# Kernel tuning notes

Hardware: AMD Instinct MI355X
Metric: run time of the kernel (lower is better)

The kernel has to match this reference:

```python
import jax, jax.numpy as jnp
import numpy as np

PAD = 7                 # init padding
T = 2 * PAD + 1         # T_side_dense = 15 shifts per axis
LAMDA = 1.0             # init lamda
EPS = 1e-16             # hardcoded epsilon in the torch loss body


def _joint_hist(x_out, x_tf_out):
    # Equivalent of F.conv2d(x_out.permute(1,0,2,3), weight=x_tf_out.permute(1,0,2,3), padding=PAD)
    # expressed as T*T shifted matmuls (correlation / cost-volume form).
    bn, k, h, w = x_out.shape
    A = jnp.transpose(x_out, (1, 0, 2, 3))      # (k, bn, h, w)  conv "input"
    B = jnp.transpose(x_tf_out, (1, 0, 2, 3))   # (k, bn, h, w)  conv "weight"
    A_pad = jnp.pad(A, ((0, 0), (0, 0), (PAD, PAD), (PAD, PAD)))

    def step(carry, s):
        dy, dx = s // T, s % T
        sl = jax.lax.dynamic_slice(A_pad, (0, 0, dy, dx), (k, bn, h, w))
        # p[n, o] at this shift = sum_{c,y,x} A_pad[n,c,y+dy,x+dx] * B[o,c,y,x]
        return carry, jnp.einsum('nchw,ochw->no', sl, B)

    _, p = jax.lax.scan(step, None, jnp.arange(T * T))
    # (T*T, k, k) -> (T, T, k, k); matches torch p_i_j.permute(2, 3, 0, 1)
    return p.reshape(T, T, k, k)


def reference(x_out, x_tf_out):
    p = _joint_hist(x_out, x_tf_out)
    # shift to positive; min is detached in torch -> stop_gradient
    p = p - jax.lax.stop_gradient(p.min()) + EPS
    # normalize per shift over the (k, k) joint
    p = p / p.sum(axis=(2, 3), keepdims=True)
    # symmetrize
    p = (p + jnp.swapaxes(p, 2, 3)) / 2.0
    p_i = p.sum(axis=2, keepdims=True)   # (T, T, 1, k) marginal (broadcasts like repeat)
    p_j = p.sum(axis=3, keepdims=True)   # (T, T, k, 1) marginal
    loss = (-p * (jnp.log(p + EPS)
                  - LAMDA * jnp.log(p_i + EPS)
                  - LAMDA * jnp.log(p_j + EPS))).sum() / (T * T)
    return loss


def setup_inputs() -> dict:
    key = jax.random.key(0)
    k1, k2 = jax.random.split(key)
    bn, k, h, w = 16, 10, 224, 224
    # simplex over axis=1 is asserted by the torch module -> use softmax
    x_out = jax.nn.softmax(jax.random.normal(k1, (bn, k, h, w), dtype=jnp.float32), axis=1)
    x_tf_out = jax.nn.softmax(jax.random.normal(k2, (bn, k, h, w), dtype=jnp.float32), axis=1)
    return {"x_out": x_out, "x_tf_out": x_tf_out}
```

## Files before the change

### kernel.cpp

```cpp
#include <hip/hip_runtime.h>
#include <stdint.h>
#include <math.h>


#define PADV 7
#define TS 15
#define KCLS 10
#define HH 224
#define WW 224
#define MD 160
#define NCELL (MD*MD)
#define NBLK 256
#define TY 14
#define BSTRIDE 232
#define BPH 240
#define PLANEE 2408
#define ABUFE (8*PLANEE)
#define NRED 400
#define LEPS 1e-16

typedef __attribute__((ext_vector_type(4))) float f32x4;
typedef __attribute__((ext_vector_type(8))) short bf16x8;

__device__ __forceinline__ unsigned short f2bf(float f) {
  union { float f; uint32_t u; } v; v.f = f;
  return (unsigned short)((v.u + 0x7FFFu + ((v.u >> 16) & 1u)) >> 16);
}

__device__ __forceinline__ uint32_t pack2bf(float a, float b) {
  return (uint32_t)f2bf(a) | ((uint32_t)f2bf(b) << 16);
}

__device__ __forceinline__ void glds16(const unsigned short* g, unsigned short* l) {
  __builtin_amdgcn_global_load_lds(
      (const __attribute__((address_space(1))) unsigned int*)g,
      (__attribute__((address_space(3))) unsigned int*)l, 16, 0, 0);
}

__device__ __forceinline__ void plane_write(const f32x4 f[4], unsigned short* awr) {
  uint32_t w[8];
#pragma unroll
  for (int k = 0; k < 8; ++k)
    w[k] = pack2bf(f[k >> 1][(k & 1) * 2], f[k >> 1][(k & 1) * 2 + 1]);
#pragma unroll
  for (int c = 0; c < 8; ++c) {
    union { uint32_t u[4]; uint4 v; } o;
    if (c & 1) {
#pragma unroll
      for (int j = 0; j < 4; ++j) o.u[j] = w[j + (c + 1) / 2];
    } else {
#pragma unroll
      for (int j = 0; j < 4; ++j)
        o.u[j] = __builtin_amdgcn_alignbit(w[j + 1 + c / 2], w[j + c / 2], 16);
    }
    *(uint4*)(awr + c * PLANEE) = o.v;
  }
}

__global__ __launch_bounds__(256)
void prep_b(const float* __restrict__ xt, unsigned short* __restrict__ bp) {
  const int idx   = blockIdx.x * 256 + threadIdx.x;
  const int rowid = idx / 29;
  const int chunk = idx - rowid * 29;
  const int x0    = chunk * 8;
  const int yy    = rowid % BPH;
  const int cls   = rowid / BPH;
  const int row   = yy - PADV;
  union { unsigned short h[8]; uint4 v; } out;
  if (row >= 0 && row < HH && chunk < 28) {
    const float4* src = (const float4*)(xt + ((size_t)cls * HH + row) * WW + x0);
    const float4 f0 = src[0], f1 = src[1];
    out.h[0] = f2bf(f0.x); out.h[1] = f2bf(f0.y);
    out.h[2] = f2bf(f0.z); out.h[3] = f2bf(f0.w);
    out.h[4] = f2bf(f1.x); out.h[5] = f2bf(f1.y);
    out.h[6] = f2bf(f1.z); out.h[7] = f2bf(f1.w);
  } else {
    out.v = make_uint4(0u, 0u, 0u, 0u);
  }
  *(uint4*)(bp + (size_t)rowid * BSTRIDE + x0) = out.v;
}

__global__ __launch_bounds__(640, 3)
void corr_gemm(const float* __restrict__ xo, const unsigned short* __restrict__ bpad,
               float* __restrict__ partials) {
  __shared__ __align__(16) unsigned short ldsA8[2 * ABUFE];
  __shared__ __align__(16) unsigned short ldsB[KCLS * 16 * BSTRIDE];

  const int tid  = threadIdx.x;
  const int bid0 = blockIdx.x;
  const int bid  = (bid0 & 7) * 32 + (bid0 >> 3);
  const int b    = bid >> 4;
  const int y0   = (bid & 15) * TY;

  const int lane = tid & 63;
  const int wv   = tid >> 6;
  const int wm   = wv >> 1;
  const int wn   = wv & 1;
  const int quad = lane >> 4;
  const int l15  = lane & 15;

  f32x4 acc[2][5];
#pragma unroll
  for (int i = 0; i < 2; ++i)
#pragma unroll
    for (int j = 0; j < 5; ++j) acc[i][j] = (f32x4){0.f, 0.f, 0.f, 0.f};

  const float* Ab = xo + (size_t)b * KCLS * HH * WW;
  const unsigned short* Bb = bpad + (size_t)b * KCLS * BPH * BSTRIDE;

  const bool aw  = tid < 300;
  const int an   = aw ? tid / 30 : 0;
  const int atp  = aw ? tid - (tid / 30) * 30 : 0;
  const int axb  = atp * 8 - 8;
  bool gv[4];
#pragma unroll
  for (int g = 0; g < 4; ++g)
    gv[g] = aw && (axb + 4 * g >= 0) && (axb + 4 * g + 4 <= WW);
  unsigned short* const awr0 = ldsA8 + an * 240 + atp * 8;

  for (int pr = wv; pr < 15 * KCLS; pr += 10) {
    const int r15  = pr / KCLS;
    const int o    = pr - r15 * KCLS;
    const int yy   = y0 + r15;
    const int slot = (y0 - PADV + r15) & 15;
    if (lane < 29)
      glds16(Bb + ((size_t)o * BPH + yy) * BSTRIDE + lane * 8,
             ldsB + (o * 16 + slot) * BSTRIDE);
  }

  f32x4 f[4];
  {
    const float* src = Ab + ((size_t)an * HH + y0) * WW + axb;
#pragma unroll
    for (int g = 0; g < 4; ++g) {
      f[g] = (f32x4){0.f, 0.f, 0.f, 0.f};
      if (gv[g]) f[g] = *(const f32x4*)(src + 4 * g);
    }
  }
  if (aw) plane_write(f, awr0);
  __syncthreads();

  int cur = 0;
  for (int s = 0; s < TY; ++s) {
    const int y = y0 + s;
    const bool more = (s + 1 < TY);

    if (more) {
      const int yy   = y + 8 + PADV;
      const int slot = (y + 8) & 15;
      if (lane < 29)
        glds16(Bb + ((size_t)wv * BPH + yy) * BSTRIDE + lane * 8,
               ldsB + (wv * 16 + slot) * BSTRIDE);
      const float* src = Ab + ((size_t)an * HH + (y + 1)) * WW + axb;
#pragma unroll
      for (int g = 0; g < 4; ++g) {
        f[g] = (f32x4){0.f, 0.f, 0.f, 0.f};
        if (gv[g]) f[g] = *(const f32x4*)(src + 4 * g);
      }
    }

    const unsigned short* paB = ldsA8 + cur * ABUFE + (l15 & 7) * PLANEE + (l15 & 8);
    const int slotB = (y + PADV - l15) & 15;

#pragma unroll 1
    for (int xc = 0; xc < 7; ++xc) {
      const int x0 = xc * 32;
      bf16x8 afrag[2], bfrag[5];
#pragma unroll
      for (int mi = 0; mi < 2; ++mi)
        afrag[mi] = *(const bf16x8*)(paB + (wm * 2 + mi) * 240 + x0 + quad * 8);
#pragma unroll
      for (int ni = 0; ni < 5; ++ni) {
        const int to = wn * 5 + ni;
        bfrag[ni] = *(const bf16x8*)(ldsB + (to * 16 + slotB) * BSTRIDE + x0 + quad * 8);
      }
#pragma unroll
      for (int mi = 0; mi < 2; ++mi)
#pragma unroll
        for (int ni = 0; ni < 5; ++ni)
          acc[mi][ni] = __builtin_amdgcn_mfma_f32_16x16x32_bf16(
              afrag[mi], bfrag[ni], acc[mi][ni], 0, 0, 0);
    }

    if (more) {
      if (aw) plane_write(f, awr0 + (cur ^ 1) * ABUFE);
      __syncthreads();
      cur ^= 1;
    }
  }

  float* outp = partials + (size_t)bid * NCELL;
#pragma unroll
  for (int mi = 0; mi < 2; ++mi)
#pragma unroll
    for (int ni = 0; ni < 5; ++ni) {
      const int mrow = (wm * 2 + mi) * 16 + quad * 4;
      const int ncol = (wn * 5 + ni) * 16 + l15;
#pragma unroll
      for (int r = 0; r < 4; ++r)
        outp[(size_t)(mrow + r) * MD + ncol] = acc[mi][ni][r];
    }
}

__global__ __launch_bounds__(256)
void reduce_all(const float* __restrict__ partials, float* __restrict__ Cout,
                float* __restrict__ mins, float* __restrict__ dout) {
  const int tid = threadIdx.x;
  const int cl  = tid & 63;
  const int g   = tid >> 6;
  const int c   = blockIdx.x * 64 + cl;
  if (blockIdx.x == 0 && tid == 0) dout[0] = 0.f;

  const float* base = partials + (size_t)g * 64 * NCELL + c;
  double s0 = 0.0, s1 = 0.0, s2 = 0.0, s3 = 0.0;
  for (int p = 0; p < 64; p += 4) {
    s0 += (double)base[(size_t)(p + 0) * NCELL];
    s1 += (double)base[(size_t)(p + 1) * NCELL];
    s2 += (double)base[(size_t)(p + 2) * NCELL];
    s3 += (double)base[(size_t)(p + 3) * NCELL];
  }
  __shared__ double redd[256];
  redd[tid] = (s0 + s1) + (s2 + s3);
  __syncthreads();

  __shared__ float redm[64];
  if (tid < 64) {
    const double tot = redd[tid] + redd[tid + 64] + redd[tid + 128] + redd[tid + 192];
    const float sf = (float)tot;
    Cout[c] = sf;
    const int m  = c / MD;
    const int nn = c - m * MD;
    const bool valid = ((m & 15) < TS) && ((nn & 15) < TS);
    redm[tid] = valid ? sf : 3.4e38f;
  }
  __syncthreads();
  for (int st = 32; st > 0; st >>= 1) {
    if (tid < st) redm[tid] = fminf(redm[tid], redm[tid + st]);
    __syncthreads();
  }
  if (tid == 0) mins[blockIdx.x] = redm[0];
}

__global__ __launch_bounds__(128)
void loss_kernel(const float* __restrict__ Cmat, const float* __restrict__ mins,
                 float* __restrict__ dout) {
  const int s   = blockIdx.x;
  const int dy  = s / TS;
  const int dx  = s - dy * TS;
  const int tid = threadIdx.x;
  __shared__ float fm[128];
  __shared__ double q[100];
  __shared__ double sym[100];
  __shared__ double pi[10], pj[10];
  __shared__ double red[128];

  {
    float v = 3.4e38f;
    for (int i = tid; i < NRED; i += 128) v = fminf(v, mins[i]);
    fm[tid] = v;
  }
  __syncthreads();
  for (int st = 64; st > 0; st >>= 1) {
    if (tid < st) fm[tid] = fminf(fm[tid], fm[tid + st]);
    __syncthreads();
  }
  const double minv = (double)fm[0];
  __syncthreads();

  if (tid < 100) {
    const int n = tid / 10, o = tid - (tid / 10) * 10;
    const double v = (double)Cmat[(size_t)(n * 16 + dx) * MD + (o * 16 + dy)];
    q[tid] = v - minv + LEPS;
  }
  __syncthreads();
  red[tid] = (tid < 100) ? q[tid] : 0.0;
  __syncthreads();
  for (int st = 64; st > 0; st >>= 1) {
    if (tid < st) red[tid] += red[tid + st];
    __syncthreads();
  }
  const double Z = red[0];
  __syncthreads();
  if (tid < 100) {
    const int n = tid / 10, o = tid - (tid / 10) * 10;
    sym[tid] = (q[n * 10 + o] + q[o * 10 + n]) * 0.5 / Z;
  }
  __syncthreads();
  if (tid < 10) {
    double a = 0.0, bsum = 0.0;
    for (int n2 = 0; n2 < 10; ++n2) {
      a    += sym[n2 * 10 + tid];
      bsum += sym[tid * 10 + n2];
    }
    pi[tid] = a;
    pj[tid] = bsum;
  }
  __syncthreads();
  double term = 0.0;
  if (tid < 100) {
    const int n = tid / 10, o = tid - (tid / 10) * 10;
    const double sp = sym[tid];
    term = -sp * (log(sp + LEPS) - log(pi[o] + LEPS) - log(pj[n] + LEPS));
  }
  red[tid] = term;
  __syncthreads();
  for (int st = 64; st > 0; st >>= 1) {
    if (tid < st) red[tid] += red[tid + st];
    __syncthreads();
  }
  if (tid == 0) atomicAdd(dout, (float)(red[0] / (double)(TS * TS)));
}

extern "C" void kernel_launch(void* const* d_in, const int* in_sizes, int n_in,
                              void* d_out, int out_size, void* d_ws, size_t ws_size,
                              hipStream_t stream) {
  const float* xo = (const float*)d_in[0];
  const float* xt = (const float*)d_in[1];
  float* ws       = (float*)d_ws;

  float* partials = ws;
  float* Cmat     = partials + (size_t)NBLK * NCELL;
  float* mins     = Cmat + NCELL;
  unsigned short* bpad = (unsigned short*)(mins + 512);
  float* out      = (float*)d_out;

  hipLaunchKernelGGL(prep_b,      dim3(4350), dim3(256), 0, stream, xt, bpad);
  hipLaunchKernelGGL(corr_gemm,   dim3(NBLK), dim3(640), 0, stream, xo, bpad, partials);
  hipLaunchKernelGGL(reduce_all,  dim3(NRED), dim3(256), 0, stream, partials, Cmat, mins, out);
  hipLaunchKernelGGL(loss_kernel, dim3(225),  dim3(128), 0, stream, Cmat, mins, out);
}
```

Baseline: 148.7 us.

## Split correlation GEMM blocks across output-class halves and single-buffer A tile

The correlation GEMM now launches twice as many blocks with half the threads, each block covering only five of the ten output classes (an N-split). Each block stages only its half of the B rows in LDS. The A plane buffer is single-buffered with an extra barrier per row, which shrinks LDS use so more blocks can be resident per CU. In exchange, every block reloads and converts the full A tile, so global reads of A double, and the added barrier serializes the A write against compute.

```diff
diff --git a/kernel.cpp b/kernel.cpp
--- a/kernel.cpp
+++ b/kernel.cpp
@@ -10,7 +10,7 @@
 #define WW 224
 #define MD 160
 #define NCELL (MD*MD)
-#define NBLK 256
+#define NGRID 256
 #define TY 14
 #define BSTRIDE 232
 #define BPH 240
@@ -80,24 +80,27 @@
   *(uint4*)(bp + (size_t)rowid * BSTRIDE + x0) = out.v;
 }
 
-__global__ __launch_bounds__(640, 3)
+#define MFMA_BF16 __builtin_amdgcn_mfma_f32_16x16x32_bf16
+
+__global__ __launch_bounds__(320)
 void corr_gemm(const float* __restrict__ xo, const unsigned short* __restrict__ bpad,
                float* __restrict__ partials) {
-  __shared__ __align__(16) unsigned short ldsA8[2 * ABUFE];
-  __shared__ __align__(16) unsigned short ldsB[KCLS * 16 * BSTRIDE];
+  __shared__ __align__(16) unsigned short ldsA8[ABUFE];
+  __shared__ __align__(16) unsigned short ldsB[5 * 16 * BSTRIDE];
 
   const int tid  = threadIdx.x;
   const int bid0 = blockIdx.x;
-  const int bid  = (bid0 & 7) * 32 + (bid0 >> 3);
-  const int b    = bid >> 4;
-  const int y0   = (bid & 15) * TY;
+  const int lb   = (bid0 & 7) * 64 + (bid0 >> 3);
+  const int b    = lb >> 5;
+  const int yg   = (lb >> 1) & 15;
+  const int nh   = lb & 1;
+  const int y0   = yg * TY;
 
   const int lane = tid & 63;
   const int wv   = tid >> 6;
-  const int wm   = wv >> 1;
-  const int wn   = wv & 1;
   const int quad = lane >> 4;
   const int l15  = lane & 15;
+  const int q8   = quad * 8;
 
   f32x4 acc[2][5];
 #pragma unroll
@@ -118,14 +121,12 @@
     gv[g] = aw && (axb + 4 * g >= 0) && (axb + 4 * g + 4 <= WW);
   unsigned short* const awr0 = ldsA8 + an * 240 + atp * 8;
 
-  for (int pr = wv; pr < 15 * KCLS; pr += 10) {
-    const int r15  = pr / KCLS;
-    const int o    = pr - r15 * KCLS;
+  for (int r15 = 0; r15 < 15; ++r15) {
     const int yy   = y0 + r15;
     const int slot = (y0 - PADV + r15) & 15;
     if (lane < 29)
-      glds16(Bb + ((size_t)o * BPH + yy) * BSTRIDE + lane * 8,
-             ldsB + (o * 16 + slot) * BSTRIDE);
+      glds16(Bb + ((size_t)(nh * 5 + wv) * BPH + yy) * BSTRIDE + lane * 8,
+             ldsB + (wv * 16 + slot) * BSTRIDE);
   }
 
   f32x4 f[4];
@@ -140,7 +141,6 @@
   if (aw) plane_write(f, awr0);
   __syncthreads();
 
-  int cur = 0;
   for (int s = 0; s < TY; ++s) {
     const int y = y0 + s;
     const bool more = (s + 1 < TY);
@@ -149,7 +149,7 @@
       const int yy   = y + 8 + PADV;
       const int slot = (y + 8) & 15;
       if (lane < 29)
-        glds16(Bb + ((size_t)wv * BPH + yy) * BSTRIDE + lane * 8,
+        glds16(Bb + ((size_t)(nh * 5 + wv) * BPH + yy) * BSTRIDE + lane * 8,
                ldsB + (wv * 16 + slot) * BSTRIDE);
       const float* src = Ab + ((size_t)an * HH + (y + 1)) * WW + axb;
 #pragma unroll
@@ -159,43 +159,40 @@
       }
     }
 
-    const unsigned short* paB = ldsA8 + cur * ABUFE + (l15 & 7) * PLANEE + (l15 & 8);
+    const unsigned short* paB = ldsA8 + (l15 & 7) * PLANEE + (l15 & 8);
     const int slotB = (y + PADV - l15) & 15;
 
 #pragma unroll 1
     for (int xc = 0; xc < 7; ++xc) {
-      const int x0 = xc * 32;
+      const int qo = xc * 32 + q8;
       bf16x8 afrag[2], bfrag[5];
 #pragma unroll
       for (int mi = 0; mi < 2; ++mi)
-        afrag[mi] = *(const bf16x8*)(paB + (wm * 2 + mi) * 240 + x0 + quad * 8);
-#pragma unroll
-      for (int ni = 0; ni < 5; ++ni) {
-        const int to = wn * 5 + ni;
-        bfrag[ni] = *(const bf16x8*)(ldsB + (to * 16 + slotB) * BSTRIDE + x0 + quad * 8);
-      }
+        afrag[mi] = *(const bf16x8*)(paB + (2 * wv + mi) * 240 + qo);
+#pragma unroll
+      for (int ni = 0; ni < 5; ++ni)
+        bfrag[ni] = *(const bf16x8*)(ldsB + (ni * 16 + slotB) * BSTRIDE + qo);
 #pragma unroll
       for (int mi = 0; mi < 2; ++mi)
 #pragma unroll
         for (int ni = 0; ni < 5; ++ni)
-          acc[mi][ni] = __builtin_amdgcn_mfma_f32_16x16x32_bf16(
-              afrag[mi], bfrag[ni], acc[mi][ni], 0, 0, 0);
+          acc[mi][ni] = MFMA_BF16(afrag[mi], bfrag[ni], acc[mi][ni], 0, 0, 0);
     }
 
     if (more) {
-      if (aw) plane_write(f, awr0 + (cur ^ 1) * ABUFE);
       __syncthreads();
-      cur ^= 1;
-    }
-  }
-
-  float* outp = partials + (size_t)bid * NCELL;
+      if (aw) plane_write(f, awr0);
+      __syncthreads();
+    }
+  }
+
+  float* outp = partials + (size_t)(b * 16 + yg) * NCELL;
 #pragma unroll
   for (int mi = 0; mi < 2; ++mi)
 #pragma unroll
     for (int ni = 0; ni < 5; ++ni) {
-      const int mrow = (wm * 2 + mi) * 16 + quad * 4;
-      const int ncol = (wn * 5 + ni) * 16 + l15;
+      const int mrow = (2 * wv + mi) * 16 + quad * 4;
+      const int ncol = (nh * 5 + ni) * 16 + l15;
 #pragma unroll
       for (int r = 0; r < 4; ++r)
         outp[(size_t)(mrow + r) * MD + ncol] = acc[mi][ni][r];
@@ -319,13 +316,13 @@
   float* ws       = (float*)d_ws;
 
   float* partials = ws;
-  float* Cmat     = partials + (size_t)NBLK * NCELL;
+  float* Cmat     = partials + (size_t)NGRID * NCELL;
   float* mins     = Cmat + NCELL;
   unsigned short* bpad = (unsigned short*)(mins + 512);
   float* out      = (float*)d_out;
 
   hipLaunchKernelGGL(prep_b,      dim3(4350), dim3(256), 0, stream, xt, bpad);
-  hipLaunchKernelGGL(corr_gemm,   dim3(NBLK), dim3(640), 0, stream, xo, bpad, partials);
+  hipLaunchKernelGGL(corr_gemm,   dim3(512),  dim3(320), 0, stream, xo, bpad, partials);
   hipLaunchKernelGGL(reduce_all,  dim3(NRED), dim3(256), 0, stream, partials, Cmat, mins, out);
   hipLaunchKernelGGL(loss_kernel, dim3(225),  dim3(128), 0, stream, Cmat, mins, out);
 }
```

Result: slower. 175.5 us (+18.1%).
